# Kernel tuning notes

Measured on AMD Instinct MI355X. Metric: run time of the kernel, lower is better.

## Reference

```python
import jax, jax.numpy as jnp
import numpy as np

BATCH, DIN, HID = 32768, 64, 1024


def setup_inputs() -> dict:
    key = jax.random.key(0)
    ks = jax.random.split(key, 8)
    s_in = 1.0 / np.sqrt(DIN)
    s_h = 1.0 / np.sqrt(HID)
    return {
        "z": jax.random.normal(ks[0], (BATCH, DIN), dtype=jnp.float32),
        # Hamiltonian net: DIN -> HID -> HID -> 1
        "W1": jax.random.normal(ks[1], (DIN, HID), dtype=jnp.float32) * s_in,
        "b1": jnp.zeros((HID,), jnp.float32),
        "W2": jax.random.normal(ks[2], (HID, HID), dtype=jnp.float32) * s_h,
        "b2": jnp.zeros((HID,), jnp.float32),
        "W3": jax.random.normal(ks[3], (HID, 1), dtype=jnp.float32) * s_h,
        "b3": jnp.zeros((1,), jnp.float32),
        # Forcing net: DIN -> HID -> DIN
        "Wf1": jax.random.normal(ks[4], (DIN, HID), dtype=jnp.float32) * s_in,
        "bf1": jnp.zeros((HID,), jnp.float32),
        "Wf2": jax.random.normal(ks[5], (HID, DIN), dtype=jnp.float32) * s_h,
        "bf2": jnp.zeros((DIN,), jnp.float32),
    }


def reference(z, W1, b1, W2, b2, W3, b3, Wf1, bf1, Wf2, bf2):
    def H_sum(zz):
        h1 = jnp.tanh(zz @ W1 + b1)          # [B, HID]
        h2 = jnp.tanh(h1 @ W2 + b2)          # [B, HID]
        return jnp.sum(h2 @ W3 + b3)         # scalar (sum of H over batch)

    gradH = jax.grad(H_sum)(z)               # [B, DIN]
    dim = z.shape[1] // 2
    # symplectic combine: dq/dt = dH/dp, dp/dt = -dH/dq
    hnn_term = jnp.concatenate([gradH[:, dim:], -gradH[:, :dim]], axis=-1)
    forcing_term = jnp.tanh(z @ Wf1 + bf1) @ Wf2 + bf2  # [B, DIN]
    return hnn_term + forcing_term
```

## Files before the change

kernel.cpp:

```cpp
#include <hip/hip_runtime.h>


typedef __attribute__((ext_vector_type(8))) short s16x8;
typedef __attribute__((ext_vector_type(4))) float f32x4;
typedef unsigned short u16;

#define DEVFN static __device__ __forceinline__

constexpr int DIN = 64;
constexpr int HID = 1024;

DEVFN u16 f2bf(float f) {
  unsigned u = __builtin_bit_cast(unsigned, f);
  u += 0x7fffu + ((u >> 16) & 1u);
  return (u16)(u >> 16);
}
DEVFN float bf2f(u16 h) {
  unsigned u = ((unsigned)h) << 16;
  return __builtin_bit_cast(float, u);
}
DEVFN float fast_tanh(float x) {
  float e = __builtin_amdgcn_exp2f(x * 2.8853900817779268f);
  return 1.0f - 2.0f * __builtin_amdgcn_rcpf(e + 1.0f);
}
DEVFN f32x4 mfma16(s16x8 a, s16x8 b, f32x4 c) {
  return __builtin_amdgcn_mfma_f32_16x16x32_bf16(a, b, c, 0, 0, 0);
}

#define GLOAD16(g, l) __builtin_amdgcn_global_load_lds( \
    (const __attribute__((address_space(1))) unsigned int*)(const void*)(g), \
    (__attribute__((address_space(3))) unsigned int*)(void*)(l), 16, 0, 0)

__global__ __launch_bounds__(256) void k0_prep(
    const float* W1, const float* W2, const float* Wf1, const float* Wf2,
    u16* W1p, u16* Wf1p, u16* W2tp, u16* W2c, u16* W1s, u16* Wf2p) {
  int id = blockIdx.x * 256 + threadIdx.x;
  {
    int n = id >> 10, k = id & 1023;
    W2tp[id] = f2bf(W2[k * HID + n]);
    W2c[id]  = f2bf(W2[id]);
  }
  if (id < 65536) {
    int n = id >> 6, k = id & 63;
    W1p[id]  = f2bf(W1[k * HID + n]);
    Wf1p[id] = f2bf(Wf1[k * HID + n]);
    int nn = id >> 10, kk2 = id & 1023;
    float s = (nn < 32) ? 1.f : -1.f;
    W1s[id]  = f2bf(s * W1[((nn + 32) & 63) * HID + kk2]);
    Wf2p[id] = f2bf(Wf2[kk2 * DIN + nn]);
  }
}

__global__ __launch_bounds__(256) void k1_h1(const float* z, const u16* Wp,
                                             const float* b, u16* o) {
  __shared__ __align__(16) u16 zl[64 * 72];
  const int tid = threadIdx.x;
  const int lane = tid & 63, w = tid >> 6;
  const int nb = blockIdx.x & 7, mb = blockIdx.x >> 3;
  const size_t m0 = (size_t)mb * 64;
  const int n0 = nb * 128;
#pragma unroll
  for (int c = 0; c < 4; ++c) {
    int i4 = c * 256 + tid;
    int row = i4 >> 4, col4 = (i4 & 15) * 4;
    f32x4 v = *reinterpret_cast<const f32x4*>(z + (m0 + row) * DIN + col4);
    u16* d = zl + row * 72 + col4;
    d[0] = f2bf(v[0]); d[1] = f2bf(v[1]); d[2] = f2bf(v[2]); d[3] = f2bf(v[3]);
  }
  __syncthreads();
  f32x4 acc[8] = {};
#pragma unroll
  for (int kk = 0; kk < 2; ++kk) {
    const int karr = kk * 32 + ((lane >> 4) << 3);
    s16x8 a = *reinterpret_cast<const s16x8*>(zl + (16 * w + (lane & 15)) * 72 + karr);
#pragma unroll
    for (int fn = 0; fn < 8; ++fn) {
      int n = n0 + fn * 16 + (lane & 15);
      s16x8 bb = *reinterpret_cast<const s16x8*>(Wp + (size_t)n * 64 + karr);
      acc[fn] = mfma16(a, bb, acc[fn]);
    }
  }
#pragma unroll
  for (int fn = 0; fn < 8; ++fn) {
    int n = n0 + fn * 16 + (lane & 15);
    float bias = b[n];
#pragma unroll
    for (int j = 0; j < 4; ++j) {
      size_t m = m0 + 16 * w + ((lane >> 4) << 2) + j;
      o[m * HID + n] = f2bf(fast_tanh(acc[fn][j] + bias));
    }
  }
}

template <int MODE>
__global__ __launch_bounds__(512, 2) void k23_gemm(
    const u16* __restrict__ A, const u16* __restrict__ Bp,
    const float* __restrict__ b2, const float* __restrict__ W3,
    const u16* __restrict__ h1in, u16* __restrict__ outb) {
  extern __shared__ u16 lds[];
  const int tid = threadIdx.x;
  const int lane = tid & 63, w = tid >> 6;
  const int wr = w >> 2, wc = w & 3;
  const int xcd = blockIdx.x & 7, local = blockIdx.x >> 3;
  const size_t m0 = (size_t)(xcd * 16 + (local >> 2)) * 256;
  const int n0 = (local & 3) * 256;

  const u16* gpa[4]; const u16* gpb[4]; int lo[4];
#pragma unroll
  for (int c = 0; c < 4; ++c) {
    int idx = c * 512 + tid, row = idx >> 3, cg = idx & 7;
    int sc = (cg ^ (row & 7)) << 3;
    gpa[c] = A + (m0 + row) * 1024 + sc;
    gpb[c] = Bp + (size_t)(n0 + row) * 1024 + sc;
    lo[c] = idx * 8;
  }
#define STAGE_A(B_, T_) { _Pragma("unroll") for (int c = 0; c < 4; ++c) \
    GLOAD16(gpa[c] + (T_) * 64, lds + (B_) * 32768 + lo[c]); }
#define STAGE_B(B_, T_) { _Pragma("unroll") for (int c = 0; c < 4; ++c) \
    GLOAD16(gpb[c] + (T_) * 64, lds + (B_) * 32768 + 16384 + lo[c]); }

  const int swz = (lane & 7) << 3;
  int aoff[8], boff[4];
#pragma unroll
  for (int i = 0; i < 8; ++i)
    aoff[i] = (wr * 128 + i * 16 + (lane & 15)) * 64 + ((lane >> 4) << 3);
#pragma unroll
  for (int j = 0; j < 4; ++j)
    boff[j] = (wc * 64 + j * 16 + (lane & 15)) * 64 + ((lane >> 4) << 3);

  f32x4 acc[8][4] = {};

#define PHASE(B_, KK_) { \
    s16x8 af[8], bf[4]; \
    _Pragma("unroll") for (int i = 0; i < 8; ++i) \
      af[i] = *reinterpret_cast<const s16x8*>(lds + (B_) * 32768 + ((aoff[i] + (KK_) * 32) ^ swz)); \
    _Pragma("unroll") for (int j = 0; j < 4; ++j) \
      bf[j] = *reinterpret_cast<const s16x8*>(lds + (B_) * 32768 + 16384 + ((boff[j] + (KK_) * 32) ^ swz)); \
    __builtin_amdgcn_s_setprio(1); \
    _Pragma("unroll") for (int i = 0; i < 8; ++i) { \
      _Pragma("unroll") for (int j = 0; j < 4; ++j) \
        acc[i][j] = mfma16(af[i], bf[j], acc[i][j]); } \
    __builtin_amdgcn_s_setprio(0); }

  STAGE_A(0, 0); STAGE_B(0, 0);
  for (int t = 0; t < 15; ++t) {
    const int cur = t & 1, nxt = cur ^ 1;
    STAGE_A(nxt, t + 1);
    asm volatile("s_waitcnt vmcnt(4)" ::: "memory");
    __builtin_amdgcn_s_barrier();
    asm volatile("" ::: "memory");
    PHASE(cur, 0);
    STAGE_B(nxt, t + 1);
    PHASE(cur, 1);
    asm volatile("" ::: "memory");
    __builtin_amdgcn_s_barrier();
    asm volatile("" ::: "memory");
  }
  asm volatile("s_waitcnt vmcnt(0)" ::: "memory");
  __builtin_amdgcn_s_barrier();
  asm volatile("" ::: "memory");
  PHASE(1, 0);
  PHASE(1, 1);
  asm volatile("" ::: "memory");
  __builtin_amdgcn_s_barrier();
  asm volatile("" ::: "memory");

  const int wbase = w * 8192;
  float b2v[4], w3v[4];
  if (MODE == 0) {
#pragma unroll
    for (int j = 0; j < 4; ++j) {
      int n = n0 + wc * 64 + j * 16 + (lane & 15);
      b2v[j] = b2[n]; w3v[j] = W3[n];
    }
  }
#pragma unroll
  for (int h = 0; h < 2; ++h) {
    if (h == 1) asm volatile("s_waitcnt lgkmcnt(0)" ::: "memory");
#pragma unroll
    for (int ip = 0; ip < 4; ++ip) {
#pragma unroll
      for (int j = 0; j < 4; ++j) {
#pragma unroll
        for (int r = 0; r < 4; ++r) {
          float v = acc[h * 4 + ip][j][r];
          u16 o;
          if (MODE == 0) {
            float tt = fast_tanh(v + b2v[j]);
            o = f2bf(w3v[j] * (1.f - tt * tt));
          } else {
            o = f2bf(v);
          }
          int lr = ip * 16 + ((lane >> 4) << 2) + r;
          lds[wbase + lr * 64 + j * 16 + (lane & 15)] = o;
        }
      }
    }
#pragma unroll
    for (int r8 = 0; r8 < 8; ++r8) {
      int lr = r8 * 8 + (lane >> 3), c8 = (lane & 7) * 8;
      s16x8 vv = *reinterpret_cast<const s16x8*>(lds + wbase + lr * 64 + c8);
      size_t grow = m0 + wr * 128 + h * 64 + lr;
      int gcol = n0 + wc * 64 + c8;
      if (MODE == 1) {
        s16x8 hh = *reinterpret_cast<const s16x8*>(h1in + grow * 1024 + gcol);
#pragma unroll
        for (int e = 0; e < 8; ++e) {
          float hv = bf2f((u16)hh[e]);
          vv[e] = (short)f2bf(bf2f((u16)vv[e]) * (1.f - hv * hv));
        }
      }
      *reinterpret_cast<s16x8*>(outb + grow * 1024 + gcol) = vv;
    }
  }
#undef STAGE_A
#undef STAGE_B
#undef PHASE
}

__global__ __launch_bounds__(256) void k4_gemm(
    const u16* __restrict__ gp1, const u16* __restrict__ f1,
    const u16* __restrict__ W1s, const u16* __restrict__ Wf2p,
    const float* __restrict__ bf2, float* __restrict__ out) {
  __shared__ __align__(16) u16 Ab[2][4096];
  __shared__ __align__(16) u16 Bb[2][4096];
  const int tid = threadIdx.x;
  const int lane = tid & 63, w = tid >> 6;
  const int lr = lane & 15, g = lane >> 4;
  const size_t m0 = (size_t)blockIdx.x * 64;

  int aoffs[2], boffs[2], lo[2];
#pragma unroll
  for (int c = 0; c < 2; ++c) {
    int idx = c * 256 + tid;
    int row = idx >> 3, cg = idx & 7;
    aoffs[c] = (int)((m0 + row) * 1024) + ((cg ^ (row & 7)) << 3);
    boffs[c] = row * 1024 + ((cg ^ (row & 7)) << 3);
    lo[c] = idx * 8;
  }
#define K4STAGE(B_, T_) { \
    const u16* ab_ = (T_) < 16 ? gp1 : f1; \
    const u16* bb_ = (T_) < 16 ? W1s : Wf2p; \
    const int ko_ = ((T_) & 15) * 64; \
    _Pragma("unroll") for (int c = 0; c < 2; ++c) { \
      GLOAD16(ab_ + aoffs[c] + ko_, Ab[B_] + lo[c]); \
      GLOAD16(bb_ + boffs[c] + ko_, Bb[B_] + lo[c]); } }

  const int arow = w * 16 + lr;
  int afr[2], bfr[2][4];
#pragma unroll
  for (int kkl = 0; kkl < 2; ++kkl) {
    afr[kkl] = arow * 64 + ((kkl * 32 + g * 8) ^ ((arow & 7) << 3));
#pragma unroll
    for (int fn = 0; fn < 4; ++fn) {
      int br = fn * 16 + lr;
      bfr[kkl][fn] = br * 64 + ((kkl * 32 + g * 8) ^ ((br & 7) << 3));
    }
  }

  f32x4 acc[4] = {};
  K4STAGE(0, 0);
  for (int t = 0; t < 31; ++t) {
    const int cur = t & 1, nxt = cur ^ 1;
    K4STAGE(nxt, t + 1);
    asm volatile("s_waitcnt vmcnt(4)" ::: "memory");
    __builtin_amdgcn_s_barrier();
    asm volatile("" ::: "memory");
#pragma unroll
    for (int kkl = 0; kkl < 2; ++kkl) {
      s16x8 a = *reinterpret_cast<const s16x8*>(Ab[cur] + afr[kkl]);
#pragma unroll
      for (int fn = 0; fn < 4; ++fn) {
        s16x8 b = *reinterpret_cast<const s16x8*>(Bb[cur] + bfr[kkl][fn]);
        acc[fn] = mfma16(a, b, acc[fn]);
      }
    }
    asm volatile("" ::: "memory");
    __builtin_amdgcn_s_barrier();
    asm volatile("" ::: "memory");
  }
  asm volatile("s_waitcnt vmcnt(0)" ::: "memory");
  __builtin_amdgcn_s_barrier();
  asm volatile("" ::: "memory");
#pragma unroll
  for (int kkl = 0; kkl < 2; ++kkl) {
    s16x8 a = *reinterpret_cast<const s16x8*>(Ab[1] + afr[kkl]);
#pragma unroll
    for (int fn = 0; fn < 4; ++fn) {
      s16x8 b = *reinterpret_cast<const s16x8*>(Bb[1] + bfr[kkl][fn]);
      acc[fn] = mfma16(a, b, acc[fn]);
    }
  }
#pragma unroll
  for (int fn = 0; fn < 4; ++fn) {
    int n = fn * 16 + lr;
    float bias = bf2[n];
#pragma unroll
    for (int j = 0; j < 4; ++j) {
      size_t m = m0 + w * 16 + g * 4 + j;
      out[m * DIN + n] = acc[fn][j] + bias;
    }
  }
#undef K4STAGE
}

extern "C" void kernel_launch(void* const* d_in, const int* in_sizes, int n_in,
                              void* d_out, int out_size, void* d_ws, size_t ws_size,
                              hipStream_t stream) {
  const float* z   = (const float*)d_in[0];
  const float* W1  = (const float*)d_in[1];
  const float* b1  = (const float*)d_in[2];
  const float* W2  = (const float*)d_in[3];
  const float* b2  = (const float*)d_in[4];
  const float* W3  = (const float*)d_in[5];
  const float* Wf1 = (const float*)d_in[7];
  const float* bf1 = (const float*)d_in[8];
  const float* Wf2 = (const float*)d_in[9];
  const float* bf2 = (const float*)d_in[10];

  char* ws = (char*)d_ws;
  u16* W1p  = (u16*)(ws + 0);
  u16* Wf1p = (u16*)(ws + 131072);
  u16* W2tp = (u16*)(ws + 262144);
  u16* W2c  = (u16*)(ws + 2359296);
  u16* W1s  = (u16*)(ws + 4456448);
  u16* Wf2p = (u16*)(ws + 4587520);
  u16* h1   = (u16*)(ws + 4718592);
  u16* gp2  = (u16*)(ws + 4718592 + 67108864);
  float* out = (float*)d_out;

  k0_prep<<<4096, 256, 0, stream>>>(W1, W2, Wf1, Wf2, W1p, Wf1p, W2tp, W2c, W1s, Wf2p);
  k1_h1<<<4096, 256, 0, stream>>>(z, W1p, b1, h1);
  k23_gemm<0><<<512, 512, 131072, stream>>>(h1, W2tp, b2, W3, nullptr, gp2);
  k23_gemm<1><<<512, 512, 131072, stream>>>(gp2, W2c, nullptr, nullptr, h1, h1);
  k1_h1<<<4096, 256, 0, stream>>>(z, Wf1p, bf1, gp2);
  k4_gemm<<<512, 256, 0, stream>>>(h1, gp2, W1s, Wf2p, bf2, out);
}
```

Measured before the change: 254.2 us.

## Restructure big GEMM main loop into quadrant-wise LDS-read/MFMA ping-pong schedule

Replaces the two-phase per-tile loop, which loaded all A/B fragments and then ran 32 MFMAs per phase, with a four-quadrant schedule. Each quadrant reads a subset of fragments from LDS and then runs 16 MFMAs, with barriers and lgkmcnt waits between steps, and both next-tile global loads are issued at the start of each tile. The aim is to cut register pressure and interleave LDS reads with MFMA across waves. In exchange it adds many more block barriers per tile and re-reads A and B fragments, which could serialise execution.

```diff
diff --git a/kernel.cpp b/kernel.cpp
--- a/kernel.cpp
+++ b/kernel.cpp
@@ -119,51 +119,55 @@
 #define STAGE_B(B_, T_) { _Pragma("unroll") for (int c = 0; c < 4; ++c) \
     GLOAD16(gpb[c] + (T_) * 64, lds + (B_) * 32768 + 16384 + lo[c]); }
 
+  const int lr15 = lane & 15, g = lane >> 4;
   const int swz = (lane & 7) << 3;
-  int aoff[8], boff[4];
-#pragma unroll
-  for (int i = 0; i < 8; ++i)
-    aoff[i] = (wr * 128 + i * 16 + (lane & 15)) * 64 + ((lane >> 4) << 3);
-#pragma unroll
-  for (int j = 0; j < 4; ++j)
-    boff[j] = (wc * 64 + j * 16 + (lane & 15)) * 64 + ((lane >> 4) << 3);
+  int aoff[2][4], boff[2][2];
+#pragma unroll
+  for (int qm = 0; qm < 2; ++qm)
+#pragma unroll
+    for (int i = 0; i < 4; ++i)
+      aoff[qm][i] = (wr * 128 + qm * 64 + i * 16 + lr15) * 64 + (g << 3);
+#pragma unroll
+  for (int qn = 0; qn < 2; ++qn)
+#pragma unroll
+    for (int j = 0; j < 2; ++j)
+      boff[qn][j] = (wc * 64 + qn * 32 + j * 16 + lr15) * 64 + (g << 3);
 
   f32x4 acc[8][4] = {};
-
-#define PHASE(B_, KK_) { \
-    s16x8 af[8], bf[4]; \
-    _Pragma("unroll") for (int i = 0; i < 8; ++i) \
-      af[i] = *reinterpret_cast<const s16x8*>(lds + (B_) * 32768 + ((aoff[i] + (KK_) * 32) ^ swz)); \
-    _Pragma("unroll") for (int j = 0; j < 4; ++j) \
-      bf[j] = *reinterpret_cast<const s16x8*>(lds + (B_) * 32768 + 16384 + ((boff[j] + (KK_) * 32) ^ swz)); \
-    __builtin_amdgcn_s_setprio(1); \
-    _Pragma("unroll") for (int i = 0; i < 8; ++i) { \
-      _Pragma("unroll") for (int j = 0; j < 4; ++j) \
-        acc[i][j] = mfma16(af[i], bf[j], acc[i][j]); } \
+  s16x8 ar[2][4], br[2][2];
+
+#define DSA(QM) { _Pragma("unroll") for (int kk = 0; kk < 2; ++kk) \
+    _Pragma("unroll") for (int i = 0; i < 4; ++i) \
+      ar[kk][i] = *reinterpret_cast<const s16x8*>(cb + ((aoff[QM][i] + kk * 32) ^ swz)); }
+#define DSB(QN) { _Pragma("unroll") for (int kk = 0; kk < 2; ++kk) \
+    _Pragma("unroll") for (int j = 0; j < 2; ++j) \
+      br[kk][j] = *reinterpret_cast<const s16x8*>(cb + 16384 + ((boff[QN][j] + kk * 32) ^ swz)); }
+#define MQ(QM, QN) { __builtin_amdgcn_s_setprio(1); \
+    _Pragma("unroll") for (int kk = 0; kk < 2; ++kk) \
+      _Pragma("unroll") for (int i = 0; i < 4; ++i) \
+        _Pragma("unroll") for (int j = 0; j < 2; ++j) \
+          acc[(QM)*4 + i][(QN)*2 + j] = mfma16(ar[kk][i], br[kk][j], acc[(QM)*4 + i][(QN)*2 + j]); \
     __builtin_amdgcn_s_setprio(0); }
+#define BAR() { asm volatile("" ::: "memory"); __builtin_amdgcn_s_barrier(); asm volatile("" ::: "memory"); }
+#define LGKM0() { asm volatile("s_waitcnt lgkmcnt(0)" ::: "memory"); __builtin_amdgcn_sched_barrier(0); }
 
   STAGE_A(0, 0); STAGE_B(0, 0);
-  for (int t = 0; t < 15; ++t) {
-    const int cur = t & 1, nxt = cur ^ 1;
-    STAGE_A(nxt, t + 1);
-    asm volatile("s_waitcnt vmcnt(4)" ::: "memory");
-    __builtin_amdgcn_s_barrier();
-    asm volatile("" ::: "memory");
-    PHASE(cur, 0);
-    STAGE_B(nxt, t + 1);
-    PHASE(cur, 1);
-    asm volatile("" ::: "memory");
-    __builtin_amdgcn_s_barrier();
-    asm volatile("" ::: "memory");
-  }
   asm volatile("s_waitcnt vmcnt(0)" ::: "memory");
-  __builtin_amdgcn_s_barrier();
-  asm volatile("" ::: "memory");
-  PHASE(1, 0);
-  PHASE(1, 1);
-  asm volatile("" ::: "memory");
-  __builtin_amdgcn_s_barrier();
-  asm volatile("" ::: "memory");
+  BAR();
+  for (int t = 0; t < 16; ++t) {
+    u16* cb = lds + (t & 1) * 32768;
+    const int nb_ = (t + 1) & 1;
+    DSA(0); DSB(0);
+    if (t < 15) { STAGE_A(nb_, t + 1); STAGE_B(nb_, t + 1); }
+    BAR(); LGKM0(); MQ(0, 0); BAR();
+    DSB(1);
+    BAR(); LGKM0(); MQ(0, 1); BAR();
+    DSA(1); DSB(0);
+    BAR(); LGKM0(); MQ(1, 0); BAR();
+    DSB(1);
+    asm volatile("s_waitcnt vmcnt(0)" ::: "memory");
+    BAR(); LGKM0(); MQ(1, 1); BAR();
+  }
 
   const int wbase = w * 8192;
   float b2v[4], w3v[4];
@@ -215,7 +219,11 @@
   }
 #undef STAGE_A
 #undef STAGE_B
-#undef PHASE
+#undef DSA
+#undef DSB
+#undef MQ
+#undef BAR
+#undef LGKM0
 }
 
 __global__ __launch_bounds__(256) void k4_gemm(
```

Result: slower. 272.6 us (+7.2%).

## Tile W2 transpose via LDS and load k4 B operand straight into registers

Applied to the files above, without the earlier changes.

Splits the weight-prep kernel so W2 conversion and transpose go through a padded LDS tile, giving coalesced reads and writes instead of strided global reads. The small weight conversions move to a separate, smaller launch. The final k4 GEMM now loads the B operand (W1s/Wf2p) directly from global into double-buffered registers, and keeps only A in a 4-deep LDS ring, prefetching two stages ahead with one barrier per step. This adds a kernel launch and raises register pressure, and the B loads into registers are uncoalesced per lane.

```diff
diff --git a/kernel.cpp b/kernel.cpp
--- a/kernel.cpp
+++ b/kernel.cpp
@@ -31,24 +31,40 @@
     (const __attribute__((address_space(1))) unsigned int*)(const void*)(g), \
     (__attribute__((address_space(3))) unsigned int*)(void*)(l), 16, 0, 0)
 
-__global__ __launch_bounds__(256) void k0_prep(
-    const float* W1, const float* W2, const float* Wf1, const float* Wf2,
-    u16* W1p, u16* Wf1p, u16* W2tp, u16* W2c, u16* W1s, u16* Wf2p) {
+__global__ __launch_bounds__(256) void k0_w2(const float* __restrict__ W2,
+                                             u16* __restrict__ W2tp, u16* __restrict__ W2c) {
+  __shared__ u16 tl[64 * 65];
+  const int bi = blockIdx.x >> 4, bj = blockIdx.x & 15;
+  const int tid = threadIdx.x;
+#pragma unroll
+  for (int i = 0; i < 16; ++i) {
+    int idx = i * 256 + tid;
+    int r = idx >> 6, c = idx & 63;
+    float v = W2[(size_t)(bi * 64 + r) * 1024 + bj * 64 + c];
+    u16 b = f2bf(v);
+    W2c[(size_t)(bi * 64 + r) * 1024 + bj * 64 + c] = b;
+    tl[r * 65 + c] = b;
+  }
+  __syncthreads();
+#pragma unroll
+  for (int i = 0; i < 16; ++i) {
+    int idx = i * 256 + tid;
+    int r = idx >> 6, c = idx & 63;
+    W2tp[(size_t)(bj * 64 + r) * 1024 + bi * 64 + c] = tl[c * 65 + r];
+  }
+}
+
+__global__ __launch_bounds__(256) void k0_small(
+    const float* W1, const float* Wf1, const float* Wf2,
+    u16* W1p, u16* Wf1p, u16* W1s, u16* Wf2p) {
   int id = blockIdx.x * 256 + threadIdx.x;
-  {
-    int n = id >> 10, k = id & 1023;
-    W2tp[id] = f2bf(W2[k * HID + n]);
-    W2c[id]  = f2bf(W2[id]);
-  }
-  if (id < 65536) {
-    int n = id >> 6, k = id & 63;
-    W1p[id]  = f2bf(W1[k * HID + n]);
-    Wf1p[id] = f2bf(Wf1[k * HID + n]);
-    int nn = id >> 10, kk2 = id & 1023;
-    float s = (nn < 32) ? 1.f : -1.f;
-    W1s[id]  = f2bf(s * W1[((nn + 32) & 63) * HID + kk2]);
-    Wf2p[id] = f2bf(Wf2[kk2 * DIN + nn]);
-  }
+  int n = id >> 6, k = id & 63;
+  W1p[id]  = f2bf(W1[k * HID + n]);
+  Wf1p[id] = f2bf(Wf1[k * HID + n]);
+  int nn = id >> 10, kk2 = id & 1023;
+  float s = (nn < 32) ? 1.f : -1.f;
+  W1s[id]  = f2bf(s * W1[((nn + 32) & 63) * HID + kk2]);
+  Wf2p[id] = f2bf(Wf2[kk2 * DIN + nn]);
 }
 
 __global__ __launch_bounds__(256) void k1_h1(const float* z, const u16* Wp,
@@ -222,75 +238,57 @@
     const u16* __restrict__ gp1, const u16* __restrict__ f1,
     const u16* __restrict__ W1s, const u16* __restrict__ Wf2p,
     const float* __restrict__ bf2, float* __restrict__ out) {
-  __shared__ __align__(16) u16 Ab[2][4096];
-  __shared__ __align__(16) u16 Bb[2][4096];
+  __shared__ __align__(16) u16 Ab[4][4096];
   const int tid = threadIdx.x;
   const int lane = tid & 63, w = tid >> 6;
   const int lr = lane & 15, g = lane >> 4;
   const size_t m0 = (size_t)blockIdx.x * 64;
 
-  int aoffs[2], boffs[2], lo[2];
+  int aoffs[2], lo[2];
 #pragma unroll
   for (int c = 0; c < 2; ++c) {
     int idx = c * 256 + tid;
     int row = idx >> 3, cg = idx & 7;
     aoffs[c] = (int)((m0 + row) * 1024) + ((cg ^ (row & 7)) << 3);
-    boffs[c] = row * 1024 + ((cg ^ (row & 7)) << 3);
     lo[c] = idx * 8;
   }
-#define K4STAGE(B_, T_) { \
-    const u16* ab_ = (T_) < 16 ? gp1 : f1; \
-    const u16* bb_ = (T_) < 16 ? W1s : Wf2p; \
-    const int ko_ = ((T_) & 15) * 64; \
-    _Pragma("unroll") for (int c = 0; c < 2; ++c) { \
-      GLOAD16(ab_ + aoffs[c] + ko_, Ab[B_] + lo[c]); \
-      GLOAD16(bb_ + boffs[c] + ko_, Bb[B_] + lo[c]); } }
+#define K4SA(T_) { const u16* ab_ = (T_) < 16 ? gp1 : f1; const int ko_ = ((T_) & 15) * 64; \
+    _Pragma("unroll") for (int c = 0; c < 2; ++c) GLOAD16(ab_ + aoffs[c] + ko_, Ab[(T_) & 3] + lo[c]); }
+#define K4LB(BR_, T_) { const u16* bb_ = (T_) < 16 ? W1s : Wf2p; const int ko_ = ((T_) & 15) * 64; \
+    _Pragma("unroll") for (int kk = 0; kk < 2; ++kk) \
+      _Pragma("unroll") for (int fn = 0; fn < 4; ++fn) \
+        BR_[kk][fn] = *reinterpret_cast<const s16x8*>(bb_ + (size_t)(fn * 16 + lr) * 1024 + ko_ + kk * 32 + g * 8); }
 
   const int arow = w * 16 + lr;
-  int afr[2], bfr[2][4];
-#pragma unroll
-  for (int kkl = 0; kkl < 2; ++kkl) {
+  int afr[2];
+#pragma unroll
+  for (int kkl = 0; kkl < 2; ++kkl)
     afr[kkl] = arow * 64 + ((kkl * 32 + g * 8) ^ ((arow & 7) << 3));
-#pragma unroll
-    for (int fn = 0; fn < 4; ++fn) {
-      int br = fn * 16 + lr;
-      bfr[kkl][fn] = br * 64 + ((kkl * 32 + g * 8) ^ ((br & 7) << 3));
-    }
-  }
-
+
+  s16x8 bA[2][4], bB[2][4];
   f32x4 acc[4] = {};
-  K4STAGE(0, 0);
-  for (int t = 0; t < 31; ++t) {
-    const int cur = t & 1, nxt = cur ^ 1;
-    K4STAGE(nxt, t + 1);
-    asm volatile("s_waitcnt vmcnt(4)" ::: "memory");
-    __builtin_amdgcn_s_barrier();
-    asm volatile("" ::: "memory");
-#pragma unroll
-    for (int kkl = 0; kkl < 2; ++kkl) {
-      s16x8 a = *reinterpret_cast<const s16x8*>(Ab[cur] + afr[kkl]);
-#pragma unroll
-      for (int fn = 0; fn < 4; ++fn) {
-        s16x8 b = *reinterpret_cast<const s16x8*>(Bb[cur] + bfr[kkl][fn]);
-        acc[fn] = mfma16(a, b, acc[fn]);
-      }
-    }
-    asm volatile("" ::: "memory");
-    __builtin_amdgcn_s_barrier();
-    asm volatile("" ::: "memory");
-  }
+
+#define K4MM(BR_, T_) { \
+    asm volatile("" ::: "memory"); __builtin_amdgcn_s_barrier(); asm volatile("" ::: "memory"); \
+    _Pragma("unroll") for (int kkl = 0; kkl < 2; ++kkl) { \
+      s16x8 a = *reinterpret_cast<const s16x8*>(Ab[(T_) & 3] + afr[kkl]); \
+      _Pragma("unroll") for (int fn = 0; fn < 4; ++fn) \
+        acc[fn] = mfma16(a, BR_[kkl][fn], acc[fn]); } }
+
+  K4LB(bA, 0); K4SA(0); K4SA(1);
+#pragma unroll 2
+  for (int t = 0; t < 30; ++t) {
+    if (t & 1) { K4LB(bA, t + 1); } else { K4LB(bB, t + 1); }
+    K4SA(t + 2);
+    asm volatile("s_waitcnt vmcnt(12)" ::: "memory");
+    if (t & 1) { K4MM(bB, t); } else { K4MM(bA, t); }
+  }
+  K4LB(bB, 31);
+  asm volatile("s_waitcnt vmcnt(10)" ::: "memory");
+  K4MM(bA, 30);
   asm volatile("s_waitcnt vmcnt(0)" ::: "memory");
-  __builtin_amdgcn_s_barrier();
-  asm volatile("" ::: "memory");
-#pragma unroll
-  for (int kkl = 0; kkl < 2; ++kkl) {
-    s16x8 a = *reinterpret_cast<const s16x8*>(Ab[1] + afr[kkl]);
-#pragma unroll
-    for (int fn = 0; fn < 4; ++fn) {
-      s16x8 b = *reinterpret_cast<const s16x8*>(Bb[1] + bfr[kkl][fn]);
-      acc[fn] = mfma16(a, b, acc[fn]);
-    }
-  }
+  K4MM(bB, 31);
+
 #pragma unroll
   for (int fn = 0; fn < 4; ++fn) {
     int n = fn * 16 + lr;
@@ -301,7 +299,9 @@
       out[m * DIN + n] = acc[fn][j] + bias;
     }
   }
-#undef K4STAGE
+#undef K4SA
+#undef K4LB
+#undef K4MM
 }
 
 extern "C" void kernel_launch(void* const* d_in, const int* in_sizes, int n_in,
@@ -329,7 +329,8 @@
   u16* gp2  = (u16*)(ws + 4718592 + 67108864);
   float* out = (float*)d_out;
 
-  k0_prep<<<4096, 256, 0, stream>>>(W1, W2, Wf1, Wf2, W1p, Wf1p, W2tp, W2c, W1s, Wf2p);
+  k0_w2<<<256, 256, 0, stream>>>(W2, W2tp, W2c);
+  k0_small<<<256, 256, 0, stream>>>(W1, Wf1, Wf2, W1p, Wf1p, W1s, Wf2p);
   k1_h1<<<4096, 256, 0, stream>>>(z, W1p, b1, h1);
   k23_gemm<0><<<512, 512, 131072, stream>>>(h1, W2tp, b2, W3, nullptr, gp2);
   k23_gemm<1><<<512, 512, 131072, stream>>>(gp2, W2c, nullptr, nullptr, h1, h1);
```

New measurement: 294.4 us. 15.8% more time.
